# Kernel tuning notes

Measured on AMD Instinct MI355X. Metric: run time of the kernel, lower is better.

Reference implementation:

```python
import jax, jax.numpy as jnp
import numpy as np

B, T, C = 2, 2048, 1024
H, D = 16, 64
SCALE = D ** -0.5


def setup_inputs() -> dict:
    key = jax.random.key(0)
    k1, k2, k3 = jax.random.split(key, 3)
    hidden_states = jax.random.normal(k1, (B, T, C), dtype=jnp.float32)
    # rotary tables: standard RoPE angles, shape (T, D//2)
    inv_freq = 1.0 / (10000.0 ** (np.arange(0, D, 2, dtype=np.float32) / D))
    ang = np.arange(T, dtype=np.float32)[:, None] * inv_freq[None, :]
    cos = jnp.asarray(np.cos(ang))
    sin = jnp.asarray(np.sin(ang))
    qkv_w = jax.random.normal(k2, (3 * H * D, C), dtype=jnp.float32) * 0.02
    qkv_b = jnp.zeros((3 * H * D,), dtype=jnp.float32)
    proj_w = jax.random.normal(k3, (C, H * D), dtype=jnp.float32) * 0.02
    proj_b = jnp.zeros((C,), dtype=jnp.float32)
    return dict(hidden_states=hidden_states, cos=cos, sin=sin,
                qkv_w=qkv_w, qkv_b=qkv_b, proj_w=proj_w, proj_b=proj_b)


def _rotary(x, cos, sin):
    # x: (B, H, T, D); cos/sin: (T, D//2) broadcast over batch and heads
    c = cos[None, None, :, :]
    s = sin[None, None, :, :]
    x1, x2 = x[..., ::2], x[..., 1::2]
    return jnp.concatenate([x1 * c - x2 * s, x1 * s + x2 * c], axis=-1)


def reference(hidden_states, cos, sin, qkv_w, qkv_b, proj_w, proj_b):
    b, t, c = hidden_states.shape
    qkv = hidden_states @ qkv_w.T + qkv_b          # (B, T, 3*H*D)
    q, k, v = jnp.split(qkv, 3, axis=-1)
    # (B, T, H, D) -> (B, H, T, D)
    q = q.reshape(b, t, H, D).transpose(0, 2, 1, 3)
    k = k.reshape(b, t, H, D).transpose(0, 2, 1, 3)
    v = v.reshape(b, t, H, D).transpose(0, 2, 1, 3)
    q = _rotary(q, cos, sin)
    k = _rotary(k, cos, sin)
    scores = jnp.einsum('bhqd,bhkd->bhqk', q, k) * SCALE
    # causal mask: -inf above the diagonal
    mask = jnp.triu(jnp.full((t, t), -jnp.inf, dtype=scores.dtype), k=1)
    scores = scores + mask[None, None, :, :]
    attn = jax.nn.softmax(scores, axis=-1)
    out = jnp.einsum('bhqk,bhkd->bhqd', attn, v)   # (B, H, T, D)
    out = out.transpose(0, 2, 1, 3).reshape(b, t, c)
    return out @ proj_w.T + proj_b
```

## Files before the change

### kernel.cpp

```cpp
#include <hip/hip_runtime.h>
#include <stdint.h>

#define B_ 2
#define T_ 2048
#define C_ 1024
#define H_ 16
#define D_ 64
#define SCALE_L2E 0.1803368801111244f

typedef unsigned short ushort_t;
typedef __attribute__((ext_vector_type(8))) __bf16 bf16x8;
typedef __attribute__((ext_vector_type(4))) float f32x4;
typedef __attribute__((ext_vector_type(4))) unsigned short ushort4_t;

__device__ __forceinline__ float bf2f(ushort_t u) {
    union { unsigned int u; float f; } v; v.u = ((unsigned int)u) << 16; return v.f;
}
__device__ __forceinline__ ushort_t f2bf(float f) {
    union { __bf16 h; ushort_t u; } v; v.h = (__bf16)f; return v.u;
}

__device__ __forceinline__ void gl16(const void* g, void* l) {
    __builtin_amdgcn_global_load_lds(
        (const __attribute__((address_space(1))) void*)g,
        (__attribute__((address_space(3))) void*)l, 16, 0, 0);
}

__device__ __forceinline__ f32x4 mfma16(bf16x8 a, bf16x8 b, f32x4 c) {
    return __builtin_amdgcn_mfma_f32_16x16x32_bf16(a, b, c, 0, 0, 0);
}

__global__ __launch_bounds__(256) void cvt3_kernel(const float* __restrict__ a, ushort_t* __restrict__ oa, int na,
                                                   const float* __restrict__ b, ushort_t* __restrict__ ob, int nb,
                                                   const float* __restrict__ c, ushort_t* __restrict__ oc, int nc) {
    int total4 = (na + nb + nc) >> 2;
    int stride = gridDim.x * blockDim.x;
    for (int i = blockIdx.x * blockDim.x + threadIdx.x; i < total4; i += stride) {
        int e = i << 2;
        const float* src; ushort_t* dst; int off;
        if (e < na) { src = a; dst = oa; off = e; }
        else if (e < na + nb) { src = b; dst = ob; off = e - na; }
        else { src = c; dst = oc; off = e - na - nb; }
        float4 v = *(const float4*)(src + off);
        ushort4_t o;
        o.x = f2bf(v.x); o.y = f2bf(v.y); o.z = f2bf(v.z); o.w = f2bf(v.w);
        *(ushort4_t*)(dst + off) = o;
    }
}

__global__ __launch_bounds__(256) void gemm_proj(const ushort_t* __restrict__ A,
                                                 const ushort_t* __restrict__ Bw,
                                                 const float* __restrict__ bias,
                                                 float* __restrict__ outf,
                                                 int M, int N, int K, int nxt) {
    int q = gridDim.x >> 3;
    int nid = (blockIdx.x & 7) * q + (blockIdx.x >> 3);
    int bx = nid % nxt, by = nid / nxt;

    __shared__ ushort_t sm[16384];
    int tid = threadIdx.x, w = tid >> 6, lane = tid & 63;
    int lr = lane >> 4, lc = lane & 15;
    int wr = w >> 1, wc = w & 1;
    int row0 = by * 128, col0 = bx * 128;

    f32x4 acc[4][4];
#pragma unroll
    for (int mf = 0; mf < 4; ++mf)
#pragma unroll
        for (int nf = 0; nf < 4; ++nf) acc[mf][nf] = (f32x4){0.f, 0.f, 0.f, 0.f};

    auto stageg = [&](int buf, int k0) {
#pragma unroll
        for (int j = 0; j < 2; ++j) {
            int idx = j * 256 + tid;
            int r = idx >> 2, c = (idx & 3) * 8;
            gl16(A + (size_t)(row0 + r) * K + k0 + c, &sm[buf * 8192 + idx * 8]);
            gl16(Bw + (size_t)(col0 + r) * K + k0 + c, &sm[buf * 8192 + 4096 + idx * 8]);
        }
    };

    stageg(0, 0);
    asm volatile("s_waitcnt vmcnt(0)" ::: "memory");
    __builtin_amdgcn_s_barrier();

    for (int k0 = 0; k0 < K; k0 += 32) {
        int cur = (k0 >> 5) & 1;
        if (k0 + 32 < K) stageg(cur ^ 1, k0 + 32);
        const ushort_t* As = &sm[cur * 8192];
        const ushort_t* Bs = &sm[cur * 8192 + 4096];
        bf16x8 af[4], bfr[4];
#pragma unroll
        for (int mf = 0; mf < 4; ++mf)
            af[mf] = *(const bf16x8*)&As[(wr * 64 + mf * 16 + lc) * 32 + 8 * lr];
#pragma unroll
        for (int nf = 0; nf < 4; ++nf)
            bfr[nf] = *(const bf16x8*)&Bs[(wc * 64 + nf * 16 + lc) * 32 + 8 * lr];
        __builtin_amdgcn_s_setprio(1);
#pragma unroll
        for (int mf = 0; mf < 4; ++mf)
#pragma unroll
            for (int nf = 0; nf < 4; ++nf)
                acc[mf][nf] = mfma16(af[mf], bfr[nf], acc[mf][nf]);
        __builtin_amdgcn_s_setprio(0);
        asm volatile("s_waitcnt vmcnt(0)" ::: "memory");
        __builtin_amdgcn_s_barrier();
    }
#pragma unroll
    for (int mf = 0; mf < 4; ++mf)
#pragma unroll
        for (int nf = 0; nf < 4; ++nf) {
            int col = col0 + wc * 64 + nf * 16 + lc;
            float bv = bias[col];
#pragma unroll
            for (int r = 0; r < 4; ++r) {
                int row = row0 + wr * 64 + mf * 16 + 4 * lr + r;
                outf[(size_t)row * N + col] = acc[mf][nf][r] + bv;
            }
        }
}

__global__ __launch_bounds__(256) void gemm_qkv_rope(const ushort_t* __restrict__ A,
                                                     const ushort_t* __restrict__ Bw,
                                                     const float* __restrict__ bias,
                                                     const float* __restrict__ cosT,
                                                     const float* __restrict__ sinT,
                                                     ushort_t* __restrict__ Qr,
                                                     ushort_t* __restrict__ Kr,
                                                     ushort_t* __restrict__ Vt) {
    const int K = 1024;
    int nid = (blockIdx.x & 7) * 96 + (blockIdx.x >> 3);
    int bx = nid % 24, by = nid / 24;

    __shared__ ushort_t sm[16384];
    int tid = threadIdx.x, w = tid >> 6, lane = tid & 63;
    int lr = lane >> 4, lc = lane & 15;
    int wr = w >> 1, wc = w & 1;
    int row0 = by * 128, col0 = bx * 128;

    f32x4 acc[4][4];
#pragma unroll
    for (int mf = 0; mf < 4; ++mf)
#pragma unroll
        for (int nf = 0; nf < 4; ++nf) acc[mf][nf] = (f32x4){0.f, 0.f, 0.f, 0.f};

    auto stageg = [&](int buf, int k0) {
#pragma unroll
        for (int j = 0; j < 2; ++j) {
            int idx = j * 256 + tid;
            int r = idx >> 2, c = (idx & 3) * 8;
            gl16(A + (size_t)(row0 + r) * K + k0 + c, &sm[buf * 8192 + idx * 8]);
            gl16(Bw + (size_t)(col0 + r) * K + k0 + c, &sm[buf * 8192 + 4096 + idx * 8]);
        }
    };

    stageg(0, 0);
    asm volatile("s_waitcnt vmcnt(0)" ::: "memory");
    __builtin_amdgcn_s_barrier();

    for (int k0 = 0; k0 < K; k0 += 32) {
        int cur = (k0 >> 5) & 1;
        if (k0 + 32 < K) stageg(cur ^ 1, k0 + 32);
        const ushort_t* As = &sm[cur * 8192];
        const ushort_t* Bs = &sm[cur * 8192 + 4096];
        bf16x8 af[4], bfr[4];
#pragma unroll
        for (int mf = 0; mf < 4; ++mf)
            af[mf] = *(const bf16x8*)&As[(wr * 64 + mf * 16 + lc) * 32 + 8 * lr];
#pragma unroll
        for (int nf = 0; nf < 4; ++nf)
            bfr[nf] = *(const bf16x8*)&Bs[(wc * 64 + nf * 16 + lc) * 32 + 8 * lr];
        __builtin_amdgcn_s_setprio(1);
#pragma unroll
        for (int mf = 0; mf < 4; ++mf)
#pragma unroll
            for (int nf = 0; nf < 4; ++nf)
                acc[mf][nf] = mfma16(af[mf], bfr[nf], acc[mf][nf]);
        __builtin_amdgcn_s_setprio(0);
        asm volatile("s_waitcnt vmcnt(0)" ::: "memory");
        __builtin_amdgcn_s_barrier();
    }

    if (bx < 16) {
        const int typ = bx >> 3;
        ushort_t* dstb = typ ? Kr : Qr;
#pragma unroll
        for (int nf = 0; nf < 4; ++nf) {
            int fullc = col0 + wc * 64 + nf * 16 + lc;
            int gc = fullc & 1023;
            int h = gc >> 6;
            int d2 = (gc & 63) >> 1;
            int odd = gc & 1;
            float bv = bias[fullc];
#pragma unroll
            for (int mf = 0; mf < 4; ++mf)
#pragma unroll
                for (int r = 0; r < 4; ++r) {
                    int row = row0 + wr * 64 + mf * 16 + 4 * lr + r;
                    int bb = row >> 11, t = row & 2047;
                    float v = acc[mf][nf][r] + bv;
                    float pv = __shfl_xor(v, 1, 64);
                    float cth = cosT[t * 32 + d2], sth = sinT[t * 32 + d2];
                    float o = odd ? (pv * sth + v * cth) : (v * cth - pv * sth);
                    if (typ == 0) o *= SCALE_L2E;
                    int od = odd ? (d2 + 32) : d2;
                    dstb[((size_t)(bb * H_ + h) * T_ + t) * D_ + od] = f2bf(o);
                }
        }
    } else {
        int bb = row0 >> 11;
        int tb = row0 & 2047;
#pragma unroll 1
        for (int half = 0; half < 2; ++half) {
            __syncthreads();
            if (wc == half) {
#pragma unroll
                for (int nf = 0; nf < 4; ++nf) {
                    int fullc = col0 + wc * 64 + nf * 16 + lc;
                    float bv = bias[fullc];
                    int c = nf * 16 + lc;
#pragma unroll
                    for (int mf = 0; mf < 4; ++mf)
#pragma unroll
                        for (int r = 0; r < 4; ++r) {
                            int tl = wr * 64 + mf * 16 + 4 * lr + r;
                            sm[c * 136 + tl] = f2bf(acc[mf][nf][r] + bv);
                        }
                }
            }
            __syncthreads();
            int h = ((bx - 16) << 1) + half;
#pragma unroll
            for (int it = 0; it < 8; ++it) {
                int idx = it * 256 + tid;
                int c = idx >> 5, j = idx & 31;
                ushort4_t vv = *(const ushort4_t*)&sm[c * 136 + 4 * j];
                *(ushort4_t*)&Vt[((size_t)(bb * H_ + h) * D_ + c) * T_ + tb + 4 * j] = vv;
            }
        }
    }
}

__global__ __launch_bounds__(256) void attn_kernel(const ushort_t* __restrict__ Qr,
                                                   const ushort_t* __restrict__ Kr,
                                                   const ushort_t* __restrict__ Vt,
                                                   ushort_t* __restrict__ attnb) {
    int id = blockIdx.x;
    int bh = id & 31;
    int i_ = id >> 5;
    int b = bh >> 4, h = bh & 15;

    const ushort_t* Qp = Qr + (size_t)bh * T_ * D_;
    const ushort_t* Kp = Kr + (size_t)bh * T_ * D_;
    const ushort_t* Vp = Vt + (size_t)bh * D_ * T_;
    int tid = threadIdx.x, w = tid >> 6, lane = tid & 63;
    int lr = lane >> 4, lc = lane & 15;

    __shared__ ushort_t Ks[2][64 * 64];
    __shared__ ushort_t Vs[2][64 * 64];
    __shared__ ushort_t Ps[4][16 * 64];

    bf16x8 ones;
#pragma unroll
    for (int i = 0; i < 8; ++i) ones[i] = (__bf16)1.0f;

    auto stage = [&](int buf, int kt) {
        int t0 = kt * 64;
#pragma unroll
        for (int j = 0; j < 2; ++j) {
            int idx = j * 256 + tid;
            int row = idx >> 3, ch = idx & 7;
            int sch = ch ^ (row & 7);
            gl16(Kp + (size_t)(t0 + row) * D_ + sch * 8, &Ks[buf][idx * 8]);
            gl16(Vp + (size_t)row * T_ + t0 + sch * 8, &Vs[buf][idx * 8]);
        }
    };

#pragma unroll 1
    for (int pass = 0; pass < 2; ++pass) {
        int qt = pass ? (31 - i_) : i_;

        int qrow = qt * 64 + w * 16 + lc;
        bf16x8 qf0 = *(const bf16x8*)(Qp + (size_t)qrow * D_ + 8 * lr);
        bf16x8 qf1 = *(const bf16x8*)(Qp + (size_t)qrow * D_ + 32 + 8 * lr);

        float m_st[4];
        f32x4 acc[4], acc_l;
#pragma unroll
        for (int r = 0; r < 4; ++r) m_st[r] = 0.f;
#pragma unroll
        for (int f = 0; f < 4; ++f) acc[f] = (f32x4){0.f, 0.f, 0.f, 0.f};
        acc_l = (f32x4){0.f, 0.f, 0.f, 0.f};

        int qg = qt * 64 + w * 16 + 4 * lr;

        stage(0, 0);
        asm volatile("s_waitcnt vmcnt(0)" ::: "memory");
        __builtin_amdgcn_s_barrier();

        for (int kt = 0; kt <= qt; ++kt) {
            int cur = kt & 1;
            if (kt < qt) stage(cur ^ 1, kt + 1);
            int t0 = kt * 64;

            f32x4 neg_m = (f32x4){-m_st[0], -m_st[1], -m_st[2], -m_st[3]};
            f32x4 sv[4];
            __builtin_amdgcn_s_setprio(1);
#pragma unroll
            for (int f = 0; f < 4; ++f) {
                sv[f] = neg_m;
                int row = 16 * f + lc;
#pragma unroll
                for (int kk = 0; kk < 2; ++kk) {
                    bf16x8 kf = *(const bf16x8*)&Ks[cur][row * 64 + (((lr + 4 * kk) ^ (row & 7)) * 8)];
                    sv[f] = mfma16(kk ? qf1 : qf0, kf, sv[f]);
                }
            }
            __builtin_amdgcn_s_setprio(0);

            float lmax[4] = {-1e30f, -1e30f, -1e30f, -1e30f};
            if (kt == qt) {
#pragma unroll
                for (int f = 0; f < 4; ++f) {
                    int kcol = t0 + 16 * f + lc;
#pragma unroll
                    for (int r = 0; r < 4; ++r) {
                        float v = sv[f][r];
                        v = (kcol > qg + r) ? -1e30f : v;
                        sv[f][r] = v;
                        lmax[r] = fmaxf(lmax[r], v);
                    }
                }
            } else {
#pragma unroll
                for (int f = 0; f < 4; ++f)
#pragma unroll
                    for (int r = 0; r < 4; ++r)
                        lmax[r] = fmaxf(lmax[r], sv[f][r]);
            }

            float dmax = fmaxf(fmaxf(lmax[0], lmax[1]), fmaxf(lmax[2], lmax[3]));
            if (!__all(dmax <= 8.0f)) {
                float tmax[4] = {lmax[0], lmax[1], lmax[2], lmax[3]};
#pragma unroll
                for (int off = 1; off < 16; off <<= 1)
#pragma unroll
                    for (int r = 0; r < 4; ++r)
                        tmax[r] = fmaxf(tmax[r], __shfl_xor(tmax[r], off, 64));
#pragma unroll
                for (int r = 0; r < 4; ++r) {
                    float d = fmaxf(tmax[r], 0.f);
                    float alpha = exp2f(-d);
                    m_st[r] += d;
                    acc_l[r] *= alpha;
#pragma unroll
                    for (int f = 0; f < 4; ++f) {
                        acc[f][r] *= alpha;
                        sv[f][r] -= d;
                    }
                }
            }

#pragma unroll
            for (int f = 0; f < 4; ++f)
#pragma unroll
                for (int r = 0; r < 4; ++r) {
                    float p = exp2f(sv[f][r]);
                    int prow = 4 * lr + r, pcol = 16 * f + lc;
                    Ps[w][prow * 64 + (((pcol >> 3) ^ (prow & 7)) * 8) + (pcol & 7)] = f2bf(p);
                }

            __builtin_amdgcn_s_setprio(1);
#pragma unroll
            for (int kk = 0; kk < 2; ++kk) {
                bf16x8 pf = *(const bf16x8*)&Ps[w][lc * 64 + (((lr + 4 * kk) ^ (lc & 7)) * 8)];
                acc_l = mfma16(pf, ones, acc_l);
#pragma unroll
                for (int f = 0; f < 4; ++f) {
                    int vrow = 16 * f + lc;
                    bf16x8 vfr = *(const bf16x8*)&Vs[cur][vrow * 64 + (((lr + 4 * kk) ^ (vrow & 7)) * 8)];
                    acc[f] = mfma16(pf, vfr, acc[f]);
                }
            }
            __builtin_amdgcn_s_setprio(0);

            asm volatile("s_waitcnt vmcnt(0)" ::: "memory");
            __builtin_amdgcn_s_barrier();
        }

        float inv[4];
#pragma unroll
        for (int r = 0; r < 4; ++r) inv[r] = 1.f / acc_l[r];
#pragma unroll
        for (int f = 0; f < 4; ++f)
#pragma unroll
            for (int r = 0; r < 4; ++r) {
                int t = qt * 64 + w * 16 + 4 * lr + r;
                attnb[((size_t)(b * T_ + t)) * 1024 + h * 64 + 16 * f + lc] =
                    f2bf(acc[f][r] * inv[r]);
            }
    }
}

extern "C" void kernel_launch(void* const* d_in, const int* in_sizes, int n_in,
                              void* d_out, int out_size, void* d_ws, size_t ws_size,
                              hipStream_t stream) {
    const float* hs     = (const float*)d_in[0];
    const float* cosp   = (const float*)d_in[1];
    const float* sinp   = (const float*)d_in[2];
    const float* qkv_w  = (const float*)d_in[3];
    const float* qkv_b  = (const float*)d_in[4];
    const float* proj_w = (const float*)d_in[5];
    const float* proj_b = (const float*)d_in[6];
    float* out = (float*)d_out;

    const int M = B_ * T_;
    ushort_t* Xb     = (ushort_t*)d_ws;
    ushort_t* Wqkvb  = Xb + (size_t)M * C_;
    ushort_t* Wprojb = Wqkvb + (size_t)3072 * C_;
    ushort_t* Qr     = Wprojb + (size_t)C_ * C_;
    ushort_t* Kr     = Qr + (size_t)B_ * H_ * T_ * D_;
    ushort_t* Vt     = Kr + (size_t)B_ * H_ * T_ * D_;
    ushort_t* attnb  = Vt + (size_t)B_ * H_ * T_ * D_;

    cvt3_kernel<<<2048, 256, 0, stream>>>(hs, Xb, M * C_,
                                          qkv_w, Wqkvb, 3072 * C_,
                                          proj_w, Wprojb, C_ * C_);

    gemm_qkv_rope<<<768, 256, 0, stream>>>(Xb, Wqkvb, qkv_b, cosp, sinp, Qr, Kr, Vt);

    attn_kernel<<<512, 256, 0, stream>>>(Qr, Kr, Vt, attnb);

    gemm_proj<<<256, 256, 0, stream>>>(attnb, Wprojb, proj_b, out, M, C_, C_, 1024 / 128);
}
```

Measured before the change: 128.5 us.

## Split attention into one query tile per block and transpose score MFMA layout

The attention kernel no longer pairs two query tiles per block (i and 31-i). It now launches 1024 blocks, each handling a single query tile, and uses a new block-index mapping that staggers causal-tile lengths across heads for balance. The QK^T MFMA operands are swapped so each lane owns a single query column. This reduces the row-max to one value per lane with two shuffles, and lets P be written to LDS as packed 4-element stores. The trade-off is more blocks with uneven causal work, relying on the hardware scheduler rather than explicit pairing, plus extra shuffles to redistribute the rescale factors.

```diff
diff --git a/kernel.cpp b/kernel.cpp
--- a/kernel.cpp
+++ b/kernel.cpp
@@ -245,8 +245,15 @@
                                                    const ushort_t* __restrict__ Vt,
                                                    ushort_t* __restrict__ attnb) {
     int id = blockIdx.x;
-    int bh = id & 31;
-    int i_ = id >> 5;
+    int x = id & 7;
+    int c = (id >> 3) & 31;
+    int g = id >> 8;
+    int bh = x + 8 * g;
+    int qt;
+    if (g == 0) qt = c;
+    else if (g == 1) qt = 31 - c;
+    else if (g == 2) qt = (c + 16) & 31;
+    else qt = 31 - ((c + 16) & 31);
     int b = bh >> 4, h = bh & 15;
 
     const ushort_t* Qp = Qr + (size_t)bh * T_ * D_;
@@ -275,130 +282,119 @@
         }
     };
 
-#pragma unroll 1
-    for (int pass = 0; pass < 2; ++pass) {
-        int qt = pass ? (31 - i_) : i_;
-
-        int qrow = qt * 64 + w * 16 + lc;
-        bf16x8 qf0 = *(const bf16x8*)(Qp + (size_t)qrow * D_ + 8 * lr);
-        bf16x8 qf1 = *(const bf16x8*)(Qp + (size_t)qrow * D_ + 32 + 8 * lr);
-
-        float m_st[4];
-        f32x4 acc[4], acc_l;
-#pragma unroll
-        for (int r = 0; r < 4; ++r) m_st[r] = 0.f;
-#pragma unroll
-        for (int f = 0; f < 4; ++f) acc[f] = (f32x4){0.f, 0.f, 0.f, 0.f};
-        acc_l = (f32x4){0.f, 0.f, 0.f, 0.f};
-
-        int qg = qt * 64 + w * 16 + 4 * lr;
-
-        stage(0, 0);
+    int qrow = qt * 64 + w * 16 + lc;
+    bf16x8 qf0 = *(const bf16x8*)(Qp + (size_t)qrow * D_ + 8 * lr);
+    bf16x8 qf1 = *(const bf16x8*)(Qp + (size_t)qrow * D_ + 32 + 8 * lr);
+
+    float m_s = 0.f;
+    f32x4 acc[4], acc_l;
+#pragma unroll
+    for (int f = 0; f < 4; ++f) acc[f] = (f32x4){0.f, 0.f, 0.f, 0.f};
+    acc_l = (f32x4){0.f, 0.f, 0.f, 0.f};
+
+    stage(0, 0);
+    asm volatile("s_waitcnt vmcnt(0)" ::: "memory");
+    __builtin_amdgcn_s_barrier();
+
+    for (int kt = 0; kt <= qt; ++kt) {
+        int cur = kt & 1;
+        if (kt < qt) stage(cur ^ 1, kt + 1);
+        int t0 = kt * 64;
+
+        f32x4 sv[4];
+        __builtin_amdgcn_s_setprio(1);
+#pragma unroll
+        for (int f = 0; f < 4; ++f) {
+            sv[f] = (f32x4){-m_s, -m_s, -m_s, -m_s};
+            int row = 16 * f + lc;
+#pragma unroll
+            for (int kk = 0; kk < 2; ++kk) {
+                bf16x8 kf = *(const bf16x8*)&Ks[cur][row * 64 + (((lr + 4 * kk) ^ (row & 7)) * 8)];
+                sv[f] = mfma16(kf, kk ? qf1 : qf0, sv[f]);
+            }
+        }
+        __builtin_amdgcn_s_setprio(0);
+
+        float lm = -1e30f;
+        if (kt == qt) {
+#pragma unroll
+            for (int f = 0; f < 4; ++f)
+#pragma unroll
+                for (int r = 0; r < 4; ++r) {
+                    int kg = t0 + 16 * f + 4 * lr + r;
+                    float v = sv[f][r];
+                    v = (kg > qrow) ? -1e30f : v;
+                    sv[f][r] = v;
+                    lm = fmaxf(lm, v);
+                }
+        } else {
+#pragma unroll
+            for (int f = 0; f < 4; ++f)
+#pragma unroll
+                for (int r = 0; r < 4; ++r)
+                    lm = fmaxf(lm, sv[f][r]);
+        }
+
+        if (!__all(lm <= 8.0f)) {
+            float tm = fmaxf(lm, __shfl_xor(lm, 16, 64));
+            tm = fmaxf(tm, __shfl_xor(tm, 32, 64));
+            float d = fmaxf(tm, 0.f);
+            m_s += d;
+            float alpha = exp2f(-d);
+            float ar[4];
+#pragma unroll
+            for (int r = 0; r < 4; ++r) ar[r] = __shfl(alpha, 4 * lr + r, 64);
+#pragma unroll
+            for (int r = 0; r < 4; ++r) {
+                acc_l[r] *= ar[r];
+#pragma unroll
+                for (int f = 0; f < 4; ++f) acc[f][r] *= ar[f == 0 ? r : r];
+            }
+#pragma unroll
+            for (int f = 0; f < 4; ++f)
+#pragma unroll
+                for (int r = 0; r < 4; ++r) sv[f][r] -= d;
+        }
+
+#pragma unroll
+        for (int f = 0; f < 4; ++f) {
+            ushort4_t pk;
+            pk.x = f2bf(exp2f(sv[f][0]));
+            pk.y = f2bf(exp2f(sv[f][1]));
+            pk.z = f2bf(exp2f(sv[f][2]));
+            pk.w = f2bf(exp2f(sv[f][3]));
+            *(ushort4_t*)&Ps[w][lc * 64 + (((4 * f + lr) ^ (lc & 14)) << 2)] = pk;
+        }
+
+        __builtin_amdgcn_s_setprio(1);
+#pragma unroll
+        for (int kk = 0; kk < 2; ++kk) {
+            bf16x8 pf = *(const bf16x8*)&Ps[w][lc * 64 + (((8 * kk + 2 * lr) ^ (lc & 14)) << 2)];
+            acc_l = mfma16(pf, ones, acc_l);
+#pragma unroll
+            for (int f = 0; f < 4; ++f) {
+                int vrow = 16 * f + lc;
+                bf16x8 vfr = *(const bf16x8*)&Vs[cur][vrow * 64 + (((lr + 4 * kk) ^ (vrow & 7)) * 8)];
+                acc[f] = mfma16(pf, vfr, acc[f]);
+            }
+        }
+        __builtin_amdgcn_s_setprio(0);
+
         asm volatile("s_waitcnt vmcnt(0)" ::: "memory");
         __builtin_amdgcn_s_barrier();
-
-        for (int kt = 0; kt <= qt; ++kt) {
-            int cur = kt & 1;
-            if (kt < qt) stage(cur ^ 1, kt + 1);
-            int t0 = kt * 64;
-
-            f32x4 neg_m = (f32x4){-m_st[0], -m_st[1], -m_st[2], -m_st[3]};
-            f32x4 sv[4];
-            __builtin_amdgcn_s_setprio(1);
-#pragma unroll
-            for (int f = 0; f < 4; ++f) {
-                sv[f] = neg_m;
-                int row = 16 * f + lc;
-#pragma unroll
-                for (int kk = 0; kk < 2; ++kk) {
-                    bf16x8 kf = *(const bf16x8*)&Ks[cur][row * 64 + (((lr + 4 * kk) ^ (row & 7)) * 8)];
-                    sv[f] = mfma16(kk ? qf1 : qf0, kf, sv[f]);
-                }
-            }
-            __builtin_amdgcn_s_setprio(0);
-
-            float lmax[4] = {-1e30f, -1e30f, -1e30f, -1e30f};
-            if (kt == qt) {
-#pragma unroll
-                for (int f = 0; f < 4; ++f) {
-                    int kcol = t0 + 16 * f + lc;
-#pragma unroll
-                    for (int r = 0; r < 4; ++r) {
-                        float v = sv[f][r];
-                        v = (kcol > qg + r) ? -1e30f : v;
-                        sv[f][r] = v;
-                        lmax[r] = fmaxf(lmax[r], v);
-                    }
-                }
-            } else {
-#pragma unroll
-                for (int f = 0; f < 4; ++f)
-#pragma unroll
-                    for (int r = 0; r < 4; ++r)
-                        lmax[r] = fmaxf(lmax[r], sv[f][r]);
-            }
-
-            float dmax = fmaxf(fmaxf(lmax[0], lmax[1]), fmaxf(lmax[2], lmax[3]));
-            if (!__all(dmax <= 8.0f)) {
-                float tmax[4] = {lmax[0], lmax[1], lmax[2], lmax[3]};
-#pragma unroll
-                for (int off = 1; off < 16; off <<= 1)
-#pragma unroll
-                    for (int r = 0; r < 4; ++r)
-                        tmax[r] = fmaxf(tmax[r], __shfl_xor(tmax[r], off, 64));
-#pragma unroll
-                for (int r = 0; r < 4; ++r) {
-                    float d = fmaxf(tmax[r], 0.f);
-                    float alpha = exp2f(-d);
-                    m_st[r] += d;
-                    acc_l[r] *= alpha;
-#pragma unroll
-                    for (int f = 0; f < 4; ++f) {
-                        acc[f][r] *= alpha;
-                        sv[f][r] -= d;
-                    }
-                }
-            }
-
-#pragma unroll
-            for (int f = 0; f < 4; ++f)
-#pragma unroll
-                for (int r = 0; r < 4; ++r) {
-                    float p = exp2f(sv[f][r]);
-                    int prow = 4 * lr + r, pcol = 16 * f + lc;
-                    Ps[w][prow * 64 + (((pcol >> 3) ^ (prow & 7)) * 8) + (pcol & 7)] = f2bf(p);
-                }
-
-            __builtin_amdgcn_s_setprio(1);
-#pragma unroll
-            for (int kk = 0; kk < 2; ++kk) {
-                bf16x8 pf = *(const bf16x8*)&Ps[w][lc * 64 + (((lr + 4 * kk) ^ (lc & 7)) * 8)];
-                acc_l = mfma16(pf, ones, acc_l);
-#pragma unroll
-                for (int f = 0; f < 4; ++f) {
-                    int vrow = 16 * f + lc;
-                    bf16x8 vfr = *(const bf16x8*)&Vs[cur][vrow * 64 + (((lr + 4 * kk) ^ (vrow & 7)) * 8)];
-                    acc[f] = mfma16(pf, vfr, acc[f]);
-                }
-            }
-            __builtin_amdgcn_s_setprio(0);
-
-            asm volatile("s_waitcnt vmcnt(0)" ::: "memory");
-            __builtin_amdgcn_s_barrier();
-        }
-
-        float inv[4];
-#pragma unroll
-        for (int r = 0; r < 4; ++r) inv[r] = 1.f / acc_l[r];
-#pragma unroll
-        for (int f = 0; f < 4; ++f)
-#pragma unroll
-            for (int r = 0; r < 4; ++r) {
-                int t = qt * 64 + w * 16 + 4 * lr + r;
-                attnb[((size_t)(b * T_ + t)) * 1024 + h * 64 + 16 * f + lc] =
-                    f2bf(acc[f][r] * inv[r]);
-            }
     }
+
+    float inv[4];
+#pragma unroll
+    for (int r = 0; r < 4; ++r) inv[r] = 1.f / acc_l[r];
+#pragma unroll
+    for (int f = 0; f < 4; ++f)
+#pragma unroll
+        for (int r = 0; r < 4; ++r) {
+            int t = qt * 64 + w * 16 + 4 * lr + r;
+            attnb[((size_t)(b * T_ + t)) * 1024 + h * 64 + 16 * f + lc] =
+                f2bf(acc[f][r] * inv[r]);
+        }
 }
 
 extern "C" void kernel_launch(void* const* d_in, const int* in_sizes, int n_in,
@@ -428,7 +424,7 @@
 
     gemm_qkv_rope<<<768, 256, 0, stream>>>(Xb, Wqkvb, qkv_b, cosp, sinp, Qr, Kr, Vt);
 
-    attn_kernel<<<512, 256, 0, stream>>>(Qr, Kr, Vt, attnb);
+    attn_kernel<<<1024, 256, 0, stream>>>(Qr, Kr, Vt, attnb);
 
     gemm_proj<<<256, 256, 0, stream>>>(attnb, Wprojb, proj_b, out, M, C_, C_, 1024 / 128);
 }
```

Measured after the change: 129.1 us. No clear change (+0.5%).

## Process two adjacent query tiles per attention block sharing K/V stages

Applied to the files above, without the earlier changes.

Each attention block now handles 128 consecutive query rows as two 64-row tiles in a single K/V sweep, instead of two separate passes over tiles i and 31-i. Every staged K/V tile and barrier is therefore shared by both query tiles. The score MFMA is transposed so that keys run along rows, which lets the max reduction use two cross-lane shuffles and lets P be written as packed 4-wide stores. The block-to-(head, tile) mapping is also remapped to group heads and to balance the causal workload. In exchange, register pressure roughly doubles for the accumulators, and the first tile's work is predicated off on the last K step.

```diff
diff --git a/kernel.cpp b/kernel.cpp
--- a/kernel.cpp
+++ b/kernel.cpp
@@ -245,8 +245,10 @@
                                                    const ushort_t* __restrict__ Vt,
                                                    ushort_t* __restrict__ attnb) {
     int id = blockIdx.x;
-    int bh = id & 31;
-    int i_ = id >> 5;
+    int lo = id & 255, hi = id >> 8;
+    int x = lo & 7, cc = lo >> 3;
+    int bh = x + 8 * (cc & 3);
+    int s = hi ? (15 - (cc >> 2)) : (cc >> 2);
     int b = bh >> 4, h = bh & 15;
 
     const ushort_t* Qp = Qr + (size_t)bh * T_ * D_;
@@ -257,7 +259,7 @@
 
     __shared__ ushort_t Ks[2][64 * 64];
     __shared__ ushort_t Vs[2][64 * 64];
-    __shared__ ushort_t Ps[4][16 * 64];
+    __shared__ ushort_t Ps[4][2][16 * 64];
 
     bf16x8 ones;
 #pragma unroll
@@ -275,130 +277,176 @@
         }
     };
 
-#pragma unroll 1
-    for (int pass = 0; pass < 2; ++pass) {
-        int qt = pass ? (31 - i_) : i_;
-
-        int qrow = qt * 64 + w * 16 + lc;
-        bf16x8 qf0 = *(const bf16x8*)(Qp + (size_t)qrow * D_ + 8 * lr);
-        bf16x8 qf1 = *(const bf16x8*)(Qp + (size_t)qrow * D_ + 32 + 8 * lr);
-
-        float m_st[4];
-        f32x4 acc[4], acc_l;
-#pragma unroll
-        for (int r = 0; r < 4; ++r) m_st[r] = 0.f;
-#pragma unroll
-        for (int f = 0; f < 4; ++f) acc[f] = (f32x4){0.f, 0.f, 0.f, 0.f};
-        acc_l = (f32x4){0.f, 0.f, 0.f, 0.f};
-
-        int qg = qt * 64 + w * 16 + 4 * lr;
-
-        stage(0, 0);
+    int q0 = s * 128 + w * 16;
+    bf16x8 qa0 = *(const bf16x8*)(Qp + (size_t)(q0 + lc) * D_ + 8 * lr);
+    bf16x8 qa1 = *(const bf16x8*)(Qp + (size_t)(q0 + lc) * D_ + 32 + 8 * lr);
+    bf16x8 qb0 = *(const bf16x8*)(Qp + (size_t)(q0 + 64 + lc) * D_ + 8 * lr);
+    bf16x8 qb1 = *(const bf16x8*)(Qp + (size_t)(q0 + 64 + lc) * D_ + 32 + 8 * lr);
+
+    float m0 = 0.f, m1 = 0.f;
+    f32x4 acc0[4], acc1[4], l0, l1;
+#pragma unroll
+    for (int f = 0; f < 4; ++f) {
+        acc0[f] = (f32x4){0.f, 0.f, 0.f, 0.f};
+        acc1[f] = (f32x4){0.f, 0.f, 0.f, 0.f};
+    }
+    l0 = (f32x4){0.f, 0.f, 0.f, 0.f};
+    l1 = (f32x4){0.f, 0.f, 0.f, 0.f};
+
+    int nkt = 2 * s + 2;
+
+    stage(0, 0);
+    asm volatile("s_waitcnt vmcnt(0)" ::: "memory");
+    __builtin_amdgcn_s_barrier();
+
+    for (int kt = 0; kt < nkt; ++kt) {
+        int cur = kt & 1;
+        if (kt + 1 < nkt) stage(cur ^ 1, kt + 1);
+        bool has0 = (kt <= 2 * s);
+        bool d0t = (kt == 2 * s);
+        bool d1t = (kt == nkt - 1);
+
+        f32x4 sv0[4], sv1[4];
+        __builtin_amdgcn_s_setprio(1);
+#pragma unroll
+        for (int f = 0; f < 4; ++f) {
+            sv0[f] = (f32x4){-m0, -m0, -m0, -m0};
+            sv1[f] = (f32x4){-m1, -m1, -m1, -m1};
+            int row = 16 * f + lc;
+#pragma unroll
+            for (int kk = 0; kk < 2; ++kk) {
+                bf16x8 kf = *(const bf16x8*)&Ks[cur][row * 64 + (((lr + 4 * kk) ^ (row & 7)) * 8)];
+                if (has0) sv0[f] = mfma16(kf, kk ? qa1 : qa0, sv0[f]);
+                sv1[f] = mfma16(kf, kk ? qb1 : qb0, sv1[f]);
+            }
+        }
+        __builtin_amdgcn_s_setprio(0);
+
+        if (d0t) {
+#pragma unroll
+            for (int f = 0; f < 4; ++f)
+#pragma unroll
+                for (int r = 0; r < 4; ++r)
+                    if (16 * f + 4 * lr + r > w * 16 + lc) sv0[f][r] = -1e30f;
+        }
+        if (d1t) {
+#pragma unroll
+            for (int f = 0; f < 4; ++f)
+#pragma unroll
+                for (int r = 0; r < 4; ++r)
+                    if (16 * f + 4 * lr + r > w * 16 + lc) sv1[f][r] = -1e30f;
+        }
+
+        float lm0 = -1e30f, lm1 = -1e30f;
+        if (has0) {
+#pragma unroll
+            for (int f = 0; f < 4; ++f)
+#pragma unroll
+                for (int r = 0; r < 4; ++r) lm0 = fmaxf(lm0, sv0[f][r]);
+        }
+#pragma unroll
+        for (int f = 0; f < 4; ++f)
+#pragma unroll
+            for (int r = 0; r < 4; ++r) lm1 = fmaxf(lm1, sv1[f][r]);
+
+        if (!__all(fmaxf(lm0, lm1) <= 8.0f)) {
+            {
+                float tm = fmaxf(lm0, __shfl_xor(lm0, 16, 64));
+                tm = fmaxf(tm, __shfl_xor(tm, 32, 64));
+                float d = fmaxf(tm, 0.f);
+                m0 += d;
+                float al = exp2f(-d);
+                float ar[4];
+#pragma unroll
+                for (int r = 0; r < 4; ++r) ar[r] = __shfl(al, 4 * lr + r, 64);
+#pragma unroll
+                for (int r = 0; r < 4; ++r) {
+                    l0[r] *= ar[r];
+#pragma unroll
+                    for (int f = 0; f < 4; ++f) acc0[f][r] *= ar[r];
+                }
+#pragma unroll
+                for (int f = 0; f < 4; ++f)
+#pragma unroll
+                    for (int r = 0; r < 4; ++r) sv0[f][r] -= d;
+            }
+            {
+                float tm = fmaxf(lm1, __shfl_xor(lm1, 16, 64));
+                tm = fmaxf(tm, __shfl_xor(tm, 32, 64));
+                float d = fmaxf(tm, 0.f);
+                m1 += d;
+                float al = exp2f(-d);
+                float ar[4];
+#pragma unroll
+                for (int r = 0; r < 4; ++r) ar[r] = __shfl(al, 4 * lr + r, 64);
+#pragma unroll
+                for (int r = 0; r < 4; ++r) {
+                    l1[r] *= ar[r];
+#pragma unroll
+                    for (int f = 0; f < 4; ++f) acc1[f][r] *= ar[r];
+                }
+#pragma unroll
+                for (int f = 0; f < 4; ++f)
+#pragma unroll
+                    for (int r = 0; r < 4; ++r) sv1[f][r] -= d;
+            }
+        }
+
+        if (has0) {
+#pragma unroll
+            for (int f = 0; f < 4; ++f) {
+                ushort4_t pk;
+                pk.x = f2bf(exp2f(sv0[f][0]));
+                pk.y = f2bf(exp2f(sv0[f][1]));
+                pk.z = f2bf(exp2f(sv0[f][2]));
+                pk.w = f2bf(exp2f(sv0[f][3]));
+                *(ushort4_t*)&Ps[w][0][lc * 64 + (((4 * f + lr) ^ (lc & 14)) << 2)] = pk;
+            }
+        }
+#pragma unroll
+        for (int f = 0; f < 4; ++f) {
+            ushort4_t pk;
+            pk.x = f2bf(exp2f(sv1[f][0]));
+            pk.y = f2bf(exp2f(sv1[f][1]));
+            pk.z = f2bf(exp2f(sv1[f][2]));
+            pk.w = f2bf(exp2f(sv1[f][3]));
+            *(ushort4_t*)&Ps[w][1][lc * 64 + (((4 * f + lr) ^ (lc & 14)) << 2)] = pk;
+        }
+
+        __builtin_amdgcn_s_setprio(1);
+#pragma unroll
+        for (int kk = 0; kk < 2; ++kk) {
+            bf16x8 pf0 = *(const bf16x8*)&Ps[w][0][lc * 64 + (((8 * kk + 2 * lr) ^ (lc & 14)) << 2)];
+            bf16x8 pf1 = *(const bf16x8*)&Ps[w][1][lc * 64 + (((8 * kk + 2 * lr) ^ (lc & 14)) << 2)];
+            if (has0) l0 = mfma16(pf0, ones, l0);
+            l1 = mfma16(pf1, ones, l1);
+#pragma unroll
+            for (int f = 0; f < 4; ++f) {
+                int vrow = 16 * f + lc;
+                bf16x8 vfr = *(const bf16x8*)&Vs[cur][vrow * 64 + (((lr + 4 * kk) ^ (vrow & 7)) * 8)];
+                if (has0) acc0[f] = mfma16(pf0, vfr, acc0[f]);
+                acc1[f] = mfma16(pf1, vfr, acc1[f]);
+            }
+        }
+        __builtin_amdgcn_s_setprio(0);
+
         asm volatile("s_waitcnt vmcnt(0)" ::: "memory");
         __builtin_amdgcn_s_barrier();
-
-        for (int kt = 0; kt <= qt; ++kt) {
-            int cur = kt & 1;
-            if (kt < qt) stage(cur ^ 1, kt + 1);
-            int t0 = kt * 64;
-
-            f32x4 neg_m = (f32x4){-m_st[0], -m_st[1], -m_st[2], -m_st[3]};
-            f32x4 sv[4];
-            __builtin_amdgcn_s_setprio(1);
-#pragma unroll
-            for (int f = 0; f < 4; ++f) {
-                sv[f] = neg_m;
-                int row = 16 * f + lc;
-#pragma unroll
-                for (int kk = 0; kk < 2; ++kk) {
-                    bf16x8 kf = *(const bf16x8*)&Ks[cur][row * 64 + (((lr + 4 * kk) ^ (row & 7)) * 8)];
-                    sv[f] = mfma16(kk ? qf1 : qf0, kf, sv[f]);
-                }
-            }
-            __builtin_amdgcn_s_setprio(0);
-
-            float lmax[4] = {-1e30f, -1e30f, -1e30f, -1e30f};
-            if (kt == qt) {
-#pragma unroll
-                for (int f = 0; f < 4; ++f) {
-                    int kcol = t0 + 16 * f + lc;
-#pragma unroll
-                    for (int r = 0; r < 4; ++r) {
-                        float v = sv[f][r];
-                        v = (kcol > qg + r) ? -1e30f : v;
-                        sv[f][r] = v;
-                        lmax[r] = fmaxf(lmax[r], v);
-                    }
-                }
-            } else {
-#pragma unroll
-                for (int f = 0; f < 4; ++f)
-#pragma unroll
-                    for (int r = 0; r < 4; ++r)
-                        lmax[r] = fmaxf(lmax[r], sv[f][r]);
-            }
-
-            float dmax = fmaxf(fmaxf(lmax[0], lmax[1]), fmaxf(lmax[2], lmax[3]));
-            if (!__all(dmax <= 8.0f)) {
-                float tmax[4] = {lmax[0], lmax[1], lmax[2], lmax[3]};
-#pragma unroll
-                for (int off = 1; off < 16; off <<= 1)
-#pragma unroll
-                    for (int r = 0; r < 4; ++r)
-                        tmax[r] = fmaxf(tmax[r], __shfl_xor(tmax[r], off, 64));
-#pragma unroll
-                for (int r = 0; r < 4; ++r) {
-                    float d = fmaxf(tmax[r], 0.f);
-                    float alpha = exp2f(-d);
-                    m_st[r] += d;
-                    acc_l[r] *= alpha;
-#pragma unroll
-                    for (int f = 0; f < 4; ++f) {
-                        acc[f][r] *= alpha;
-                        sv[f][r] -= d;
-                    }
-                }
-            }
-
-#pragma unroll
-            for (int f = 0; f < 4; ++f)
-#pragma unroll
-                for (int r = 0; r < 4; ++r) {
-                    float p = exp2f(sv[f][r]);
-                    int prow = 4 * lr + r, pcol = 16 * f + lc;
-                    Ps[w][prow * 64 + (((pcol >> 3) ^ (prow & 7)) * 8) + (pcol & 7)] = f2bf(p);
-                }
-
-            __builtin_amdgcn_s_setprio(1);
-#pragma unroll
-            for (int kk = 0; kk < 2; ++kk) {
-                bf16x8 pf = *(const bf16x8*)&Ps[w][lc * 64 + (((lr + 4 * kk) ^ (lc & 7)) * 8)];
-                acc_l = mfma16(pf, ones, acc_l);
-#pragma unroll
-                for (int f = 0; f < 4; ++f) {
-                    int vrow = 16 * f + lc;
-                    bf16x8 vfr = *(const bf16x8*)&Vs[cur][vrow * 64 + (((lr + 4 * kk) ^ (vrow & 7)) * 8)];
-                    acc[f] = mfma16(pf, vfr, acc[f]);
-                }
-            }
-            __builtin_amdgcn_s_setprio(0);
-
-            asm volatile("s_waitcnt vmcnt(0)" ::: "memory");
-            __builtin_amdgcn_s_barrier();
-        }
-
-        float inv[4];
-#pragma unroll
-        for (int r = 0; r < 4; ++r) inv[r] = 1.f / acc_l[r];
-#pragma unroll
-        for (int f = 0; f < 4; ++f)
-#pragma unroll
-            for (int r = 0; r < 4; ++r) {
-                int t = qt * 64 + w * 16 + 4 * lr + r;
-                attnb[((size_t)(b * T_ + t)) * 1024 + h * 64 + 16 * f + lc] =
-                    f2bf(acc[f][r] * inv[r]);
-            }
-    }
+    }
+
+    float inv0[4], inv1[4];
+#pragma unroll
+    for (int r = 0; r < 4; ++r) { inv0[r] = 1.f / l0[r]; inv1[r] = 1.f / l1[r]; }
+#pragma unroll
+    for (int f = 0; f < 4; ++f)
+#pragma unroll
+        for (int r = 0; r < 4; ++r) {
+            int t = s * 128 + w * 16 + 4 * lr + r;
+            attnb[((size_t)(b * T_ + t)) * 1024 + h * 64 + 16 * f + lc] =
+                f2bf(acc0[f][r] * inv0[r]);
+            attnb[((size_t)(b * T_ + t + 64)) * 1024 + h * 64 + 16 * f + lc] =
+                f2bf(acc1[f][r] * inv1[r]);
+        }
 }
 
 extern "C" void kernel_launch(void* const* d_in, const int* in_sizes, int n_in,
```

Result: slower. 135.8 us (+5.6%).
